# Kernel tuning notes

Hardware: AMD Instinct MI355X
Metric: run time of the kernel (lower is better)

## Reference

```python
import jax, jax.numpy as jnp
import numpy as np

# Scalars from init_kwargs (qat_training=False inference path)
IN_ZP = 0
OUT_ZP = 0
IN_SCALE = 0.02
OUT_SCALE = 0.05
STRIDE = (1, 1)
PAD = (1, 1)      # (ph, pw); module pads (pw, pw, ph, ph) via F.pad
DIL = (1, 1)
GROUPS = 1
QMIN, QMAX = -128, 127  # get_quantized_range(8)


def setup_inputs() -> dict:
    key = jax.random.key(0)
    k1, k2, k3, k4 = jax.random.split(key, 4)
    x = jax.random.randint(k1, (32, 128, 56, 56), -128, 128, dtype=jnp.int32).astype(jnp.int8)
    weight = jax.random.randint(k2, (256, 128, 3, 3), -128, 128, dtype=jnp.int32).astype(jnp.int8)
    bias = jax.random.randint(k3, (256,), -1000, 1000, dtype=jnp.int32)
    weight_scale = jax.random.uniform(k4, (256,), minval=1e-3, maxval=1e-2, dtype=jnp.float32)
    return {"x": x, "weight": weight, "bias": bias, "weight_scale": weight_scale}


def reference(x, weight, bias, weight_scale):
    # Pad spatial dims with the input zero point (matches F.pad(..., value=input_zero_point))
    xp = jnp.pad(x.astype(jnp.int32),
                 ((0, 0), (0, 0), (PAD[0], PAD[0]), (PAD[1], PAD[1])),
                 constant_values=IN_ZP)
    # Exact int32-accumulate convolution (torch CPU path)
    acc = jax.lax.conv_general_dilated(
        xp, weight.astype(jnp.int32),
        window_strides=STRIDE, padding='VALID', rhs_dilation=DIL,
        dimension_numbers=('NCHW', 'OIHW', 'NCHW'),
        feature_group_count=GROUPS, preferred_element_type=jnp.int32)
    acc = acc + bias[None, :, None, None]
    # Per-output-channel requantization
    scale = (IN_SCALE * weight_scale / OUT_SCALE)[None, :, None, None]
    out = acc.astype(jnp.float32) * scale + OUT_ZP
    out = jnp.clip(jnp.round(out), QMIN, QMAX).astype(jnp.int8)
    return out
```

## Files before the change

kernel.cpp:

```cpp
#include <hip/hip_runtime.h>
#include <hip/hip_bf16.h>
#include <stdint.h>


#define NB   32
#define CIN  128
#define HO   56
#define WO   56
#define KOUT 256
#define HP   58
#define ROWB (HP * CIN)

typedef int v4i  __attribute__((ext_vector_type(4)));
typedef int v16i __attribute__((ext_vector_type(16)));

__global__ __launch_bounds__(256) void pack_x_kernel(const int* __restrict__ x,
                                                     int8_t* __restrict__ xp) {
  __shared__ int tile[WO][33];
  const int tid = threadIdx.x;
  const int r = blockIdx.x;
  const int n = blockIdx.y;
  const int tx = tid & 63;
  const int ty = tid >> 6;
  const bool interior = (r >= 1) && (r <= HO);

  if (interior && tx < WO) {
    const int h = r - 1;
    #pragma unroll
    for (int c0 = 0; c0 < CIN; c0 += 16) {
      const int c = c0 + ty * 4;
      const int base = ((n * CIN + c) * HO + h) * WO + tx;
      const int v0 = x[base];
      const int v1 = x[base + HO * WO];
      const int v2 = x[base + 2 * HO * WO];
      const int v3 = x[base + 3 * HO * WO];
      tile[tx][c >> 2] = (v0 & 0xff) | ((v1 & 0xff) << 8) | ((v2 & 0xff) << 16) | (v3 << 24);
    }
  }
  __syncthreads();
  #pragma unroll
  for (int it = 0; it < 8; ++it) {
    const int i = it * 256 + tid;
    if (i < HP * 32) {
      const int w = i >> 5;
      const int c4 = i & 31;
      const int v = (interior && w >= 1 && w <= WO) ? tile[w - 1][c4] : 0;
      *reinterpret_cast<int*>(xp + ((size_t)(n * HP + r) * HP + w) * CIN + c4 * 4) = v;
    }
  }
}

__global__ __launch_bounds__(256) void pack_w_kernel(const int* __restrict__ wgt,
                                                     int8_t* __restrict__ wq) {
  const int wid = blockIdx.x * 256 + threadIdx.x;
  const int wi = wid & 3;
  const int ci = wid >> 2;
  const int c   = ci & 7;
  const int nch = (ci >> 3) & 127;
  const int tt  = ci >> 10;
  const int tap = tt % 9;
  const int kt  = tt / 9;
  const int k  = kt * 128 + nch;
  const int c0 = c * 16 + wi * 4;
  const int base = (k * CIN + c0) * 9 + tap;
  const int v0 = wgt[base];
  const int v1 = wgt[base + 9];
  const int v2 = wgt[base + 18];
  const int v3 = wgt[base + 27];
  reinterpret_cast<int*>(wq)[wid] =
      (v0 & 0xff) | ((v1 & 0xff) << 8) | ((v2 & 0xff) << 16) | (v3 << 24);
}

__global__ __launch_bounds__(256, 4) void conv_kernel(const int8_t* __restrict__ xp,
                                                      const int8_t* __restrict__ wq,
                                                      const int* __restrict__ bias,
                                                      const float* __restrict__ wscale,
                                                      int* __restrict__ out) {
  __shared__ __align__(16) int8_t lx[4 * HP * 8 * 16];

  const int tid = threadIdx.x;
  const int h0 = blockIdx.x * 2;
  const int n_img = blockIdx.y;
  const int kt = blockIdx.z;

  const int lane = tid & 63;
  const int wid = tid >> 6;
  const int wm = wid & 1;
  const int wn = wid >> 1;
  const int p0 = lane & 31;
  const int half = lane >> 5;

  const int8_t* xg = xp + ((size_t)(n_img * HP) + h0) * ROWB;
  const int8_t* wbase = wq + (size_t)kt * 9216 * 16;

  #pragma unroll
  for (int it = 0; it < 8; ++it) {
    const int i = it * 256 + tid;
    if (i < 4 * HP * 8) {
      const int pf = i >> 3;
      const int cc = (i & 7) ^ (pf & 7);
      const int4 v = *reinterpret_cast<const int4*>(xg + pf * CIN + (cc << 4));
      *reinterpret_cast<int4*>(lx + i * 16) = v;
    }
  }
  __syncthreads();

  v16i acc[2][2];
  #pragma unroll
  for (int mt = 0; mt < 2; ++mt)
    #pragma unroll
    for (int nt = 0; nt < 2; ++nt)
      #pragma unroll
      for (int e = 0; e < 16; ++e) acc[mt][nt][e] = 0;

  const int base0 = wm * HP + p0;
  const int8_t* bp0 = wbase + (wn * 64 + p0) * 128 + half * 16;
  const int8_t* bp1 = bp0 + 32 * 128;

  #pragma unroll
  for (int tap = 0; tap < 9; ++tap) {
    const int kh = tap / 3, kw = tap % 3;
    const int pfb = base0 + kh * HP + kw;
    const int keya = (pfb & 7) << 4;
    const int tapoff = tap * 16384;

    #pragma unroll
    for (int ks = 0; ks < 4; ++ks) {
      const int ch = (ks * 2 + half) << 4;
      v4i a[2], b[2];
      #pragma unroll
      for (int mt = 0; mt < 2; ++mt)
        a[mt] = *reinterpret_cast<const v4i*>(lx + (pfb + mt * 32) * CIN + (ch ^ keya));
      b[0] = *reinterpret_cast<const v4i*>(bp0 + tapoff + ks * 32);
      b[1] = *reinterpret_cast<const v4i*>(bp1 + tapoff + ks * 32);
      acc[0][0] = __builtin_amdgcn_mfma_i32_32x32x32_i8(a[0], b[0], acc[0][0], 0, 0, 0);
      acc[0][1] = __builtin_amdgcn_mfma_i32_32x32x32_i8(a[0], b[1], acc[0][1], 0, 0, 0);
      acc[1][0] = __builtin_amdgcn_mfma_i32_32x32x32_i8(a[1], b[0], acc[1][0], 0, 0, 0);
      acc[1][1] = __builtin_amdgcn_mfma_i32_32x32x32_i8(a[1], b[1], acc[1][1], 0, 0, 0);
    }
  }

  const int h = h0 + wm;
  #pragma unroll
  for (int nt = 0; nt < 2; ++nt) {
    const int ch = kt * 128 + wn * 64 + nt * 32 + p0;
    const int bi = bias[ch];
    const float sc = (0.02f * wscale[ch]) / 0.05f;
    int* ob = out + (((size_t)n_img * KOUT + ch) * HO + h) * WO;
    #pragma unroll
    for (int mt = 0; mt < 2; ++mt) {
      #pragma unroll
      for (int r = 0; r < 16; ++r) {
        const int m = (r & 3) + 8 * (r >> 2) + 4 * half;
        const int w = mt * 32 + m;
        if (w < WO) {
          float v = (float)(acc[mt][nt][r] + bi) * sc;
          v = rintf(v);
          v = fminf(fmaxf(v, -128.0f), 127.0f);
          ob[w] = (int)v;
        }
      }
    }
  }
}

extern "C" void kernel_launch(void* const* d_in, const int* in_sizes, int n_in,
                              void* d_out, int out_size, void* d_ws, size_t ws_size,
                              hipStream_t stream) {
  const int* x = (const int*)d_in[0];
  const int* wgt = (const int*)d_in[1];
  const int* bias = (const int*)d_in[2];
  const float* wscale = (const float*)d_in[3];
  int* out = (int*)d_out;

  int8_t* xp = (int8_t*)d_ws;
  int8_t* wq = (int8_t*)d_ws + (size_t)NB * HP * ROWB;

  pack_x_kernel<<<dim3(HP, NB), 256, 0, stream>>>(x, xp);
  pack_w_kernel<<<288, 256, 0, stream>>>(wgt, wq);
  conv_kernel<<<dim3(28, 32, 2), 256, 0, stream>>>(xp, wq, bias, wscale, out);
}
```

Before: 226.2 us.

## Swap MFMA operands, double-buffer weight fragments in registers, coalesce output stores

Swaps the MFMA operand roles so weights are the A operand and input pixels the B operand. Each thread's accumulator rows now map to output channels and its lanes to consecutive pixels, so output stores become contiguous along width. Weight fragments for the next tap are prefetched from global memory into a two-slot register buffer while the current tap's MFMAs run, and bias and scale are staged in shared memory. Occupancy is lowered from 4 to 3 blocks per CU to make room for the extra registers, and the LDS buffer grows slightly.

```diff
diff --git a/kernel.cpp b/kernel.cpp
--- a/kernel.cpp
+++ b/kernel.cpp
@@ -71,12 +71,14 @@
       (v0 & 0xff) | ((v1 & 0xff) << 8) | ((v2 & 0xff) << 16) | (v3 << 24);
 }
 
-__global__ __launch_bounds__(256, 4) void conv_kernel(const int8_t* __restrict__ xp,
+__global__ __launch_bounds__(256, 3) void conv_kernel(const int8_t* __restrict__ xp,
                                                       const int8_t* __restrict__ wq,
                                                       const int* __restrict__ bias,
                                                       const float* __restrict__ wscale,
                                                       int* __restrict__ out) {
-  __shared__ __align__(16) int8_t lx[4 * HP * 8 * 16];
+  __shared__ __align__(16) int8_t lx[240 * CIN];
+  __shared__ int   bsh[128];
+  __shared__ float ssh[128];
 
   const int tid = threadIdx.x;
   const int h0 = blockIdx.x * 2;
@@ -85,13 +87,13 @@
 
   const int lane = tid & 63;
   const int wid = tid >> 6;
-  const int wm = wid & 1;
-  const int wn = wid >> 1;
+  const int wc = wid & 1;
+  const int wp = wid >> 1;
   const int p0 = lane & 31;
   const int half = lane >> 5;
 
   const int8_t* xg = xp + ((size_t)(n_img * HP) + h0) * ROWB;
-  const int8_t* wbase = wq + (size_t)kt * 9216 * 16;
+  const int8_t* wbase = wq + (size_t)kt * 147456;
 
   #pragma unroll
   for (int it = 0; it < 8; ++it) {
@@ -103,6 +105,11 @@
       *reinterpret_cast<int4*>(lx + i * 16) = v;
     }
   }
+  if (tid < 128) {
+    const int ch = kt * 128 + tid;
+    bsh[tid] = bias[ch];
+    ssh[tid] = (0.02f * wscale[ch]) / 0.05f;
+  }
   __syncthreads();
 
   v16i acc[2][2];
@@ -113,46 +120,56 @@
       #pragma unroll
       for (int e = 0; e < 16; ++e) acc[mt][nt][e] = 0;
 
-  const int base0 = wm * HP + p0;
-  const int8_t* bp0 = wbase + (wn * 64 + p0) * 128 + half * 16;
-  const int8_t* bp1 = bp0 + 32 * 128;
+  const int8_t* ab = wbase + (wc * 64 + p0) * 128 + half * 16;
+  const int base0 = wp * HP + p0;
+
+  v4i wf[2][8];
+  #pragma unroll
+  for (int ks = 0; ks < 4; ++ks)
+    #pragma unroll
+    for (int mt = 0; mt < 2; ++mt)
+      wf[0][ks * 2 + mt] = *reinterpret_cast<const v4i*>(ab + mt * 4096 + ks * 32);
 
   #pragma unroll
   for (int tap = 0; tap < 9; ++tap) {
+    const int cb = tap & 1, nb = cb ^ 1;
+    if (tap < 8) {
+      #pragma unroll
+      for (int ks = 0; ks < 4; ++ks)
+        #pragma unroll
+        for (int mt = 0; mt < 2; ++mt)
+          wf[nb][ks * 2 + mt] =
+              *reinterpret_cast<const v4i*>(ab + (tap + 1) * 16384 + mt * 4096 + ks * 32);
+    }
     const int kh = tap / 3, kw = tap % 3;
     const int pfb = base0 + kh * HP + kw;
     const int keya = (pfb & 7) << 4;
-    const int tapoff = tap * 16384;
 
     #pragma unroll
     for (int ks = 0; ks < 4; ++ks) {
       const int ch = (ks * 2 + half) << 4;
-      v4i a[2], b[2];
-      #pragma unroll
-      for (int mt = 0; mt < 2; ++mt)
-        a[mt] = *reinterpret_cast<const v4i*>(lx + (pfb + mt * 32) * CIN + (ch ^ keya));
-      b[0] = *reinterpret_cast<const v4i*>(bp0 + tapoff + ks * 32);
-      b[1] = *reinterpret_cast<const v4i*>(bp1 + tapoff + ks * 32);
-      acc[0][0] = __builtin_amdgcn_mfma_i32_32x32x32_i8(a[0], b[0], acc[0][0], 0, 0, 0);
-      acc[0][1] = __builtin_amdgcn_mfma_i32_32x32x32_i8(a[0], b[1], acc[0][1], 0, 0, 0);
-      acc[1][0] = __builtin_amdgcn_mfma_i32_32x32x32_i8(a[1], b[0], acc[1][0], 0, 0, 0);
-      acc[1][1] = __builtin_amdgcn_mfma_i32_32x32x32_i8(a[1], b[1], acc[1][1], 0, 0, 0);
+      const v4i pf0 = *reinterpret_cast<const v4i*>(lx + pfb * CIN + (ch ^ keya));
+      const v4i pf1 = *reinterpret_cast<const v4i*>(lx + (pfb + 32) * CIN + (ch ^ keya));
+      acc[0][0] = __builtin_amdgcn_mfma_i32_32x32x32_i8(wf[cb][ks * 2 + 0], pf0, acc[0][0], 0, 0, 0);
+      acc[0][1] = __builtin_amdgcn_mfma_i32_32x32x32_i8(wf[cb][ks * 2 + 0], pf1, acc[0][1], 0, 0, 0);
+      acc[1][0] = __builtin_amdgcn_mfma_i32_32x32x32_i8(wf[cb][ks * 2 + 1], pf0, acc[1][0], 0, 0, 0);
+      acc[1][1] = __builtin_amdgcn_mfma_i32_32x32x32_i8(wf[cb][ks * 2 + 1], pf1, acc[1][1], 0, 0, 0);
     }
   }
 
-  const int h = h0 + wm;
+  const int h = h0 + wp;
   #pragma unroll
-  for (int nt = 0; nt < 2; ++nt) {
-    const int ch = kt * 128 + wn * 64 + nt * 32 + p0;
-    const int bi = bias[ch];
-    const float sc = (0.02f * wscale[ch]) / 0.05f;
-    int* ob = out + (((size_t)n_img * KOUT + ch) * HO + h) * WO;
+  for (int mt = 0; mt < 2; ++mt) {
     #pragma unroll
-    for (int mt = 0; mt < 2; ++mt) {
+    for (int r = 0; r < 16; ++r) {
+      const int mrow = (r & 3) + 8 * (r >> 2) + 4 * half;
+      const int cl = wc * 64 + mt * 32 + mrow;
+      const int bi = bsh[cl];
+      const float sc = ssh[cl];
+      int* ob = out + (((size_t)(n_img * KOUT + kt * 128 + cl)) * HO + h) * WO;
       #pragma unroll
-      for (int r = 0; r < 16; ++r) {
-        const int m = (r & 3) + 8 * (r >> 2) + 4 * half;
-        const int w = mt * 32 + m;
+      for (int nt = 0; nt < 2; ++nt) {
+        const int w = nt * 32 + p0;
         if (w < WO) {
           float v = (float)(acc[mt][nt][r] + bi) * sc;
           v = rintf(v);
```

After: 217.9 us. 1.04x faster.
